# Kernel tuning notes

Hardware: AMD Instinct MI355X
Metric: run time of the kernel (lower is better)

## Reference

```python
import jax, jax.numpy as jnp
import numpy as np

N, E, D, G, L = 50000, 400000, 64, 256, 4
VA, VB = 64, 8   # atom / bond feature vocab sizes
NUM_ATOM_FEATS, NUM_BOND_FEATS = 9, 3
MSG_EPS = 1e-7   # GENConv message epsilon
LN_EPS = 1e-5


def layernorm(x, g, b):
    mu = x.mean(-1, keepdims=True)
    var = x.var(-1, keepdims=True)
    return (x - mu) * jax.lax.rsqrt(var + LN_EPS) * g + b


def genconv(h, edge_emb, src, dst, W, b):
    # GENConv (aggr='softmax', t=1, mlp_layers=1):
    # msg = relu(x_j + e) + eps; per-dst per-feature softmax-weighted sum; mlp(x + m)
    msg = jax.nn.relu(h[src] + edge_emb) + MSG_EPS          # [E, D]
    mmax = jax.ops.segment_max(msg, dst, num_segments=N)    # [N, D]
    mmax = jnp.where(jnp.isfinite(mmax), mmax, 0.0)         # nodes with no in-edges
    ex = jnp.exp(msg - mmax[dst])
    denom = jax.ops.segment_sum(ex, dst, num_segments=N)
    alpha = ex / jnp.maximum(denom[dst], 1e-16)
    m = jax.ops.segment_sum(alpha * msg, dst, num_segments=N)  # [N, D]
    return (h + m) @ W + b


def setup_inputs():
    key = jax.random.key(0)
    ks = jax.random.split(key, 10)
    x = jax.random.randint(ks[0], (N, NUM_ATOM_FEATS), 0, VA)
    edge_index = jax.random.randint(ks[1], (2, E), 0, N)
    edge_attr = jax.random.randint(ks[2], (E, NUM_BOND_FEATS), 0, VB)
    batch = jnp.sort(jax.random.randint(ks[3], (N,), 0, G))
    s = 0.02
    w = 1.0 / np.sqrt(D).astype(np.float32)
    atom_emb = jax.random.normal(ks[4], (NUM_ATOM_FEATS, VA, D), jnp.float32) * s
    bond_emb = jax.random.normal(ks[5], (NUM_BOND_FEATS, VB, D), jnp.float32) * s
    gcn_W = jax.random.normal(ks[6], (L, D, D), jnp.float32) * w
    gcn_b = jnp.zeros((L, D), jnp.float32)
    norm_g = jnp.ones((L, D), jnp.float32)
    norm_b = jnp.zeros((L, D), jnp.float32)
    vn_emb = jnp.zeros((1, D), jnp.float32)  # constant-init virtualnode embedding
    vn_W1 = jax.random.normal(ks[7], (L - 1, D, D), jnp.float32) * w
    vn_b1 = jnp.zeros((L - 1, D), jnp.float32)
    vn_g1 = jnp.ones((L - 1, D), jnp.float32)
    vn_be1 = jnp.zeros((L - 1, D), jnp.float32)
    vn_W2 = jax.random.normal(ks[8], (L - 1, D, D), jnp.float32) * w
    vn_b2 = jnp.zeros((L - 1, D), jnp.float32)
    vn_g2 = jnp.ones((L - 1, D), jnp.float32)
    vn_be2 = jnp.zeros((L - 1, D), jnp.float32)
    return dict(x=x, edge_index=edge_index, edge_attr=edge_attr, batch=batch,
                atom_emb=atom_emb, bond_emb=bond_emb, gcn_W=gcn_W, gcn_b=gcn_b,
                norm_g=norm_g, norm_b=norm_b, vn_emb=vn_emb,
                vn_W1=vn_W1, vn_b1=vn_b1, vn_g1=vn_g1, vn_be1=vn_be1,
                vn_W2=vn_W2, vn_b2=vn_b2, vn_g2=vn_g2, vn_be2=vn_be2)


def reference(x, edge_index, edge_attr, batch, atom_emb, bond_emb, gcn_W, gcn_b,
              norm_g, norm_b, vn_emb, vn_W1, vn_b1, vn_g1, vn_be1,
              vn_W2, vn_b2, vn_g2, vn_be2):
    src, dst = edge_index[0], edge_index[1]
    # AtomEncoder / BondEncoder: sum of per-feature embedding lookups
    h = atom_emb[jnp.arange(NUM_ATOM_FEATS)[None, :], x].sum(1)          # [N, D]
    edge_emb = bond_emb[jnp.arange(NUM_BOND_FEATS)[None, :], edge_attr].sum(1)  # [E, D]
    vn = jnp.broadcast_to(vn_emb[0], (G, D))
    h = h + vn[batch]
    # block == 'res+' (eval mode: dropout is identity)
    h = genconv(h, edge_emb, src, dst, gcn_W[0], gcn_b[0])
    for l in range(1, L):
        h2 = jax.nn.relu(layernorm(h, norm_g[l - 1], norm_b[l - 1]))
        vt = jax.ops.segment_sum(h2, batch, num_segments=G) + vn         # global_add_pool
        vt = jax.nn.relu(layernorm(vt @ vn_W1[l - 1] + vn_b1[l - 1], vn_g1[l - 1], vn_be1[l - 1]))
        vn = jax.nn.relu(layernorm(vt @ vn_W2[l - 1] + vn_b2[l - 1], vn_g2[l - 1], vn_be2[l - 1]))
        h2 = h2 + vn[batch]
        h = genconv(h2, edge_emb, src, dst, gcn_W[l], gcn_b[l]) + h
    return layernorm(h, norm_g[L - 1], norm_b[L - 1])
```

## Files before the change

kernel.cpp:

```cpp
#include <hip/hip_runtime.h>
#include <hip/hip_bf16.h>

typedef __hip_bfloat16 bf16;

#define GNUM 256
#define LN_EPS 1e-5f
#define MSG_EPS 1e-7f

typedef float f4v __attribute__((ext_vector_type(4)));
typedef short s8v __attribute__((ext_vector_type(8)));
typedef __bf16 b8v __attribute__((ext_vector_type(8)));

template <typename V>
__device__ auto mfma_bf16_(V a, V b, f4v c, int)
    -> decltype(__builtin_amdgcn_mfma_f32_16x16x32_bf16(a, b, c, 0, 0, 0)) {
  return __builtin_amdgcn_mfma_f32_16x16x32_bf16(a, b, c, 0, 0, 0);
}
template <typename V>
__device__ f4v mfma_bf16_(V a, V b, f4v c, long) {
  return __builtin_amdgcn_mfma_f32_16x16x32_bf16(__builtin_bit_cast(s8v, a),
                                                 __builtin_bit_cast(s8v, b), c, 0, 0, 0);
}
__device__ __forceinline__ f4v mfma16(uint4 a, uint4 b, f4v c){
  return mfma_bf16_(__builtin_bit_cast(b8v, a), __builtin_bit_cast(b8v, b), c, 0);
}

__device__ __forceinline__ float bu2f(unsigned short u){
  unsigned v = ((unsigned)u) << 16; return __builtin_bit_cast(float, v);
}
__device__ __forceinline__ unsigned short f2bu(float f){
  unsigned u = __builtin_bit_cast(unsigned, f);
  return (unsigned short)((u + 0x7FFFu + ((u >> 16) & 1u)) >> 16);
}

__device__ __forceinline__ float wave_sum64(float v){
  #pragma unroll
  for (int off = 32; off > 0; off >>= 1) v += __shfl_xor(v, off, 64);
  return v;
}

struct Params15 {
  const void* src[15];
  int n[15];
  int off[15];
};

__global__ __launch_bounds__(256) void k_convert(Params15 P, int* __restrict__ flag,
                                                 float* __restrict__ dst,
                                                 int* __restrict__ counts, int nc){
  __shared__ int isf_sh;
  int tid = threadIdx.x;
  if (tid < 64){
    const unsigned short* u = (const unsigned short*)P.src[0];
    int bad = 0;
    for (int k = tid; k < 256; k += 64){
      unsigned short v = u[2*k];
      if (((v >> 7) & 0xFFu) >= 137u) bad = 1;
    }
    unsigned long long m = __ballot(bad);
    if (tid == 0) isf_sh = (m != 0ull) ? 1 : 0;
  }
  __syncthreads();
  bool isf = (isf_sh != 0);
  if (blockIdx.x == 0 && tid == 0) *flag = isf ? 1 : 0;
  for (int a = 0; a < 15; ++a){
    int n = P.n[a];
    float* d = dst + P.off[a];
    if (isf){
      const float* s = (const float*)P.src[a];
      for (int i = blockIdx.x*256 + tid; i < n; i += gridDim.x*256) d[i] = s[i];
    } else {
      const bf16* s = (const bf16*)P.src[a];
      for (int i = blockIdx.x*256 + tid; i < n; i += gridDim.x*256) d[i] = __bfloat162float(s[i]);
    }
  }
  for (int i = blockIdx.x*256 + tid; i < nc; i += gridDim.x*256) counts[i] = 0;
}

__global__ void k_count(const int* __restrict__ dst, int* __restrict__ counts, int E){
  int e = blockIdx.x*256 + threadIdx.x;
  if (e < E) atomicAdd(counts + dst[e], 1);
}

__global__ __launch_bounds__(256) void k_scan1(const int* __restrict__ counts,
                                               int* __restrict__ offs,
                                               int* __restrict__ btot, int n){
  __shared__ int wsum[4];
  int tid = threadIdx.x, w = tid >> 6, lane = tid & 63;
  int i = blockIdx.x*256 + tid;
  int v = (i < n) ? counts[i] : 0;
  int incl = v;
  #pragma unroll
  for (int off = 1; off < 64; off <<= 1){
    int t = __shfl_up(incl, off, 64);
    if (lane >= off) incl += t;
  }
  if (lane == 63) wsum[w] = incl;
  __syncthreads();
  int woff = 0;
  for (int k = 0; k < w; ++k) woff += wsum[k];
  int tot = incl + woff;
  if (i < n) offs[i+1] = tot;
  if (tid == 255) btot[blockIdx.x] = tot;
}

__global__ __launch_bounds__(256) void k_scan2(const int* __restrict__ btot,
                                               int* __restrict__ bexc, int nb){
  __shared__ int wsum[4];
  __shared__ int carry_sh;
  int tid = threadIdx.x, w = tid >> 6, lane = tid & 63;
  if (tid == 0) carry_sh = 0;
  __syncthreads();
  for (int base = 0; base < nb; base += 256){
    int i = base + tid;
    int v = (i < nb) ? btot[i] : 0;
    int incl = v;
    #pragma unroll
    for (int off = 1; off < 64; off <<= 1){
      int t = __shfl_up(incl, off, 64);
      if (lane >= off) incl += t;
    }
    if (lane == 63) wsum[w] = incl;
    __syncthreads();
    int carry = carry_sh;
    int woff = 0;
    for (int k = 0; k < w; ++k) woff += wsum[k];
    if (i < nb) bexc[i] = carry + woff + incl - v;
    __syncthreads();
    if (tid == 0) carry_sh = carry + wsum[0] + wsum[1] + wsum[2] + wsum[3];
    __syncthreads();
  }
}

__global__ void k_scan3(int* __restrict__ offs, int* __restrict__ cursor,
                        const int* __restrict__ bexc, int n){
  int i = blockIdx.x*256 + threadIdx.x;
  if (i == 0){ offs[0] = 0; cursor[0] = 0; }
  if (i < n){
    int v = offs[i+1] + bexc[blockIdx.x];
    offs[i+1] = v;
    if (i+1 < n) cursor[i+1] = v;
  }
}

__global__ void k_scatter(const int* __restrict__ src, const int* __restrict__ dst,
                          const int* __restrict__ ea, int* __restrict__ cursor,
                          int* __restrict__ payload, int E){
  int e = blockIdx.x*256 + threadIdx.x;
  if (e >= E) return;
  int d = dst[e];
  int pos = atomicAdd(cursor + d, 1);
  payload[pos] = (src[e] & 0xFFFF) | (ea[e*3] << 16) | (ea[e*3+1] << 19) | (ea[e*3+2] << 22);
}

__global__ void k_prep(const float* __restrict__ gw, unsigned short* __restrict__ Wf,
                       const int* __restrict__ batch, int* __restrict__ goffs,
                       const int* __restrict__ x, const float* __restrict__ atom_emb,
                       const float* __restrict__ vn_emb, unsigned short* __restrict__ b0,
                       int n){
  if (blockIdx.x < 64){
    int t = blockIdx.x*256 + threadIdx.x;
    int j = t & 7, lane = (t >> 3) & 63, nt = (t >> 9) & 3, kt = (t >> 11) & 1, l = t >> 12;
    int k = kt*32 + (lane >> 4)*8 + j;
    int c = nt*16 + (lane & 15);
    Wf[t] = f2bu(gw[l*4096 + k*64 + c]);
  } else if (blockIdx.x < 66){
    int g = (blockIdx.x - 64)*256 + threadIdx.x;
    if (g > GNUM) return;
    if (g == GNUM){ goffs[GNUM] = n; return; }
    int lo = 0, hi = n;
    while (lo < hi){ int mid = (lo+hi)>>1; if (batch[mid] < g) lo = mid+1; else hi = mid; }
    goffs[g] = lo;
  } else {
    int t = (blockIdx.x - 66) * 256 + threadIdx.x;
    int i = t >> 6, j = t & 63;
    if (i >= n) return;
    float acc = vn_emb[j];
    #pragma unroll
    for (int f = 0; f < 9; ++f){
      int idx = x[i*9 + f];
      acc += atom_emb[(f*64 + idx)*64 + j];
    }
    b0[t] = f2bu(acc);
  }
}

__global__ __launch_bounds__(256) void k_layer(
    const unsigned short* __restrict__ b0, const int* __restrict__ offs,
    const int* __restrict__ payload, const float* __restrict__ bond,
    const unsigned short* __restrict__ Wf, const float* __restrict__ bias,
    unsigned short* __restrict__ hres, float2* __restrict__ rowstat,
    void* __restrict__ finalout, const float* __restrict__ ng,
    const float* __restrict__ nb, const int* __restrict__ flag,
    int use_res, int mode, int n){
  __shared__ float Bs[1536];
  __shared__ __align__(16) unsigned short T[16][72];
  __shared__ float PS1[4][16], PS2[4][16];
  int tid = threadIdx.x;
  for (int idx = tid; idx < 1536; idx += 256) Bs[idx] = bond[idx];
  __syncthreads();
  int w = tid >> 6, j = tid & 63;
  int v0 = blockIdx.x * 16;
  int vb = v0 + w*4;

  int oidx = vb + (j < 5 ? j : 4);
  if (oidx > n) oidx = n;
  int o5 = offs[oidx];

  for (int r = 0; r < 4; ++r){
    int v = vb + r;
    float tv = 0.f;
    if (v < n){
      int e0 = __builtin_amdgcn_readfirstlane(__shfl(o5, r, 64));
      int e1 = __builtin_amdgcn_readfirstlane(__shfl(o5, r + 1, 64));
      float own = bu2f(b0[((unsigned)v << 6) + j]);
      tv = own;
      if (e1 > e0){
        float den = 0.f, num = 0.f;
        for (int e = e0; e < e1; e += 8){
          int rem = e1 - e;
          int pu[8]; float hv[8];
          #pragma unroll
          for (int u = 0; u < 8; ++u){
            int ei = (u < rem) ? e + u : e0;
            pu[u] = payload[ei];
          }
          #pragma unroll
          for (int u = 0; u < 8; ++u)
            hv[u] = bu2f(b0[((unsigned)(pu[u] & 0xFFFF) << 6) + j]);
          if (rem >= 8){
            #pragma unroll
            for (int u = 0; u < 8; ++u){
              int p = pu[u];
              float eev = Bs[((p >> 16) & 7)*64 + j]
                        + Bs[(8 + ((p >> 19) & 7))*64 + j]
                        + Bs[(16 + ((p >> 22) & 7))*64 + j];
              float mm = fmaxf(hv[u] + eev, 0.f) + MSG_EPS;
              float ex = __expf(mm);
              den += ex;
              num = fmaf(ex, mm, num);
            }
          } else {
            #pragma unroll
            for (int u = 0; u < 8; ++u){
              if (u < rem){
                int p = pu[u];
                float eev = Bs[((p >> 16) & 7)*64 + j]
                          + Bs[(8 + ((p >> 19) & 7))*64 + j]
                          + Bs[(16 + ((p >> 22) & 7))*64 + j];
                float mm = fmaxf(hv[u] + eev, 0.f) + MSG_EPS;
                float ex = __expf(mm);
                den += ex;
                num = fmaf(ex, mm, num);
              }
            }
          }
        }
        tv = own + num / fmaxf(den, 1e-16f);
      }
    }
    T[w*4 + r][j] = f2bu(tv);
  }
  __syncthreads();

  int ct = w;
  int quad = j >> 4, lm = j & 15;
  const uint4* Wfv = (const uint4*)Wf;
  uint4 B0 = Wfv[(size_t)(0*4 + ct)*64 + j];
  uint4 B1 = Wfv[(size_t)(1*4 + ct)*64 + j];
  uint4 A0 = *(const uint4*)&T[lm][8*quad];
  uint4 A1 = *(const uint4*)&T[lm][32 + 8*quad];
  f4v acc = (f4v){0.f,0.f,0.f,0.f};
  acc = mfma16(A0, B0, acc);
  acc = mfma16(A1, B1, acc);

  int col = ct*16 + lm;
  float bv = bias[col];
  float s1[4], s2[4];
  #pragma unroll
  for (int reg = 0; reg < 4; ++reg){
    int row = v0 + quad*4 + reg;
    float val = acc[reg] + bv;
    if (use_res && row < n) val += bu2f(hres[((unsigned)row << 6) + col]);
    acc[reg] = val;
    s1[reg] = val;
    s2[reg] = val*val;
  }
  #pragma unroll
  for (int reg = 0; reg < 4; ++reg){
    #pragma unroll
    for (int m = 1; m < 16; m <<= 1){
      s1[reg] += __shfl_xor(s1[reg], m, 64);
      s2[reg] += __shfl_xor(s2[reg], m, 64);
    }
  }
  if (lm == 0){
    #pragma unroll
    for (int reg = 0; reg < 4; ++reg){
      int rl = quad*4 + reg;
      PS1[ct][rl] = s1[reg];
      PS2[ct][rl] = s2[reg];
    }
  }
  __syncthreads();

  if (mode == 0){
    #pragma unroll
    for (int reg = 0; reg < 4; ++reg){
      int rl = quad*4 + reg;
      int row = v0 + rl;
      if (row >= n) continue;
      hres[((size_t)row << 6) + col] = f2bu(acc[reg]);
      if (ct == 0 && lm == 0){
        float t1 = PS1[0][rl] + PS1[1][rl] + PS1[2][rl] + PS1[3][rl];
        float t2 = PS2[0][rl] + PS2[1][rl] + PS2[2][rl] + PS2[3][rl];
        float mu = t1 * (1.f/64.f);
        float var = fmaxf(t2 * (1.f/64.f) - mu*mu, 0.f);
        rowstat[row] = make_float2(mu, rsqrtf(var + LN_EPS));
      }
    }
    return;
  }

  bool isf = (*flag != 0);
  #pragma unroll
  for (int reg = 0; reg < 4; ++reg){
    int rl = quad*4 + reg;
    int row = v0 + rl;
    if (row >= n) continue;
    float t1 = PS1[0][rl] + PS1[1][rl] + PS1[2][rl] + PS1[3][rl];
    float t2 = PS2[0][rl] + PS2[1][rl] + PS2[2][rl] + PS2[3][rl];
    float mu = t1 * (1.f/64.f);
    float var = fmaxf(t2 * (1.f/64.f) - mu*mu, 0.f);
    float rstd = rsqrtf(var + LN_EPS);
    float y = (acc[reg] - mu) * rstd * ng[col] + nb[col];
    size_t o = ((size_t)row << 6) + col;
    if (isf) ((float*)finalout)[o] = y;
    else     ((bf16*)finalout)[o]  = __float2bfloat16(y);
  }
}

__global__ __launch_bounds__(512) void k_vn(
    const unsigned short* __restrict__ hres, const float2* __restrict__ rowstat,
    const int* __restrict__ goffs,
    const float* __restrict__ vn_emb, float* __restrict__ vn,
    unsigned short* __restrict__ b0,
    const float* __restrict__ ng, const float* __restrict__ nbb,
    const float* __restrict__ W1, const float* __restrict__ b1,
    const float* __restrict__ g1, const float* __restrict__ be1,
    const float* __restrict__ W2, const float* __restrict__ b2,
    const float* __restrict__ g2, const float* __restrict__ be2,
    int first){
  __shared__ float Ws[4096];
  __shared__ float part[8][64];
  __shared__ float rowbuf[64];
  __shared__ float vnew[64];
  int tid = threadIdx.x, w = tid >> 6, j = tid & 63, g = blockIdx.x;
  float ngj = ng[j], nbj = nbb[j];
  for (int idx = tid; idx < 4096; idx += 512) Ws[idx] = W1[idx];
  int r0 = goffs[g], r1 = goffs[g+1];
  float sum = 0.f;
  for (int i = r0 + w; i < r1; i += 8){
    float xv = bu2f(hres[((unsigned)i << 6) + j]);
    float2 st = rowstat[i];
    sum += fmaxf((xv - st.x) * st.y * ngj + nbj, 0.f);
  }
  part[w][j] = sum;
  __syncthreads();
  float y = 0.f;
  if (tid < 64){
    float s = part[0][j] + part[1][j] + part[2][j] + part[3][j]
            + part[4][j] + part[5][j] + part[6][j] + part[7][j]
            + (first ? vn_emb[j] : vn[((unsigned)g << 6) + j]);
    rowbuf[j] = s;
  }
  __syncthreads();
  if (tid < 64){
    float acc = b1[j];
    #pragma unroll
    for (int k = 0; k < 64; ++k) acc = fmaf(rowbuf[k], Ws[k*64 + j], acc);
    float mu = wave_sum64(acc) * (1.f/64.f);
    float d = acc - mu;
    float var = wave_sum64(d*d) * (1.f/64.f);
    y = fmaxf(d * rsqrtf(var + LN_EPS) * g1[j] + be1[j], 0.f);
  }
  __syncthreads();
  for (int idx = tid; idx < 4096; idx += 512) Ws[idx] = W2[idx];
  if (tid < 64) rowbuf[j] = y;
  __syncthreads();
  if (tid < 64){
    float acc = b2[j];
    #pragma unroll
    for (int k = 0; k < 64; ++k) acc = fmaf(rowbuf[k], Ws[k*64 + j], acc);
    float mu = wave_sum64(acc) * (1.f/64.f);
    float d = acc - mu;
    float var = wave_sum64(d*d) * (1.f/64.f);
    float v2 = fmaxf(d * rsqrtf(var + LN_EPS) * g2[j] + be2[j], 0.f);
    vn[((unsigned)g << 6) + j] = v2;
    vnew[j] = v2;
  }
  __syncthreads();
  float vj = vnew[j];
  for (int i = r0 + w; i < r1; i += 8){
    float xv = bu2f(hres[((unsigned)i << 6) + j]);
    float2 st = rowstat[i];
    float h2 = fmaxf((xv - st.x) * st.y * ngj + nbj, 0.f);
    b0[((unsigned)i << 6) + j] = f2bu(h2 + vj);
  }
}

extern "C" void kernel_launch(void* const* d_in, const int* in_sizes, int n_in,
                              void* d_out, int out_size, void* d_ws, size_t ws_size,
                              hipStream_t stream){
  const int* x          = (const int*)d_in[0];
  const int* edge_index = (const int*)d_in[1];
  const int* edge_attr  = (const int*)d_in[2];
  const int* batch      = (const int*)d_in[3];

  const int N = in_sizes[3];
  const int E = in_sizes[2] / 3;
  const int L = 4;

  const int P_ATOM = 0, P_BOND = 36864, P_GW = 38400, P_GB = 54784,
            P_NG = 55040, P_NB = 55296, P_VNE = 55552, P_W1 = 55616,
            P_B1 = 67904, P_G1 = 68096, P_BE1 = 68288, P_W2 = 68480,
            P_B2 = 80768, P_G2 = 80960, P_BE2 = 81152, P_END = 81344;

  char* ws = (char*)d_ws;
  size_t off = 0;
  auto alloc = [&](size_t bytes)->char*{
    char* p = ws + off; off += (bytes + 255) & ~(size_t)255; return p;
  };
  int*    flag   = (int*)alloc(256);
  float*  par    = (float*)alloc((size_t)P_END * 4);
  unsigned short* Wf  = (unsigned short*)alloc(16384 * 2);
  unsigned short* b0  = (unsigned short*)alloc((size_t)N*64*2);
  unsigned short* hres= (unsigned short*)alloc((size_t)N*64*2);
  float2* rowstat= (float2*)alloc((size_t)N*8);
  int*    counts = (int*)alloc((size_t)N*4);
  int*    offs   = (int*)alloc((size_t)(N+1)*4);
  int*    cursor = (int*)alloc((size_t)N*4);
  int*    btot   = (int*)alloc(1024);
  int*    bexc   = (int*)alloc(1024);
  int*    payload= (int*)alloc((size_t)E*4);
  int*    goffs  = (int*)alloc((size_t)(GNUM+1)*4);
  float*  vn     = (float*)alloc((size_t)GNUM*64*4);
  (void)ws_size; (void)n_in; (void)out_size;

  Params15 P;
  const int poffs[15] = {P_ATOM,P_BOND,P_GW,P_GB,P_NG,P_NB,P_VNE,P_W1,P_B1,P_G1,P_BE1,P_W2,P_B2,P_G2,P_BE2};
  for (int a = 0; a < 15; ++a){ P.src[a] = d_in[4+a]; P.n[a] = in_sizes[4+a]; P.off[a] = poffs[a]; }

  int nodeGrid = (N*64 + 255) / 256;
  int nScanB   = (N + 255) / 256;
  int eGrid    = (E + 255) / 256;
  const int* srcp = edge_index;
  const int* dstp = edge_index + E;

  k_convert<<<128, 256, 0, stream>>>(P, flag, par, counts, N);
  k_count<<<eGrid, 256, 0, stream>>>(dstp, counts, E);
  k_scan1<<<nScanB, 256, 0, stream>>>(counts, offs, btot, N);
  k_scan2<<<1, 256, 0, stream>>>(btot, bexc, nScanB);
  k_scan3<<<nScanB, 256, 0, stream>>>(offs, cursor, bexc, N);
  k_scatter<<<eGrid, 256, 0, stream>>>(srcp, dstp, edge_attr, cursor, payload, E);
  k_prep<<<66 + nodeGrid, 256, 0, stream>>>(par + P_GW, Wf, batch, goffs,
                                            x, par + P_ATOM, par + P_VNE, b0, N);

  int layerGrid = (N + 15) / 16;
  for (int l = 0; l < L; ++l){
    if (l > 0){
      k_vn<<<GNUM, 512, 0, stream>>>(hres, rowstat, goffs, par + P_VNE, vn, b0,
                                     par + P_NG + (l-1)*64, par + P_NB + (l-1)*64,
                                     par + P_W1 + (l-1)*4096, par + P_B1 + (l-1)*64,
                                     par + P_G1 + (l-1)*64, par + P_BE1 + (l-1)*64,
                                     par + P_W2 + (l-1)*4096, par + P_B2 + (l-1)*64,
                                     par + P_G2 + (l-1)*64, par + P_BE2 + (l-1)*64,
                                     l == 1 ? 1 : 0);
    }
    int mode = (l == L-1) ? 1 : 0;
    k_layer<<<layerGrid, 256, 0, stream>>>(b0, offs, payload, par + P_BOND,
                                           Wf + (size_t)l*4096, par + P_GB + l*64,
                                           hres, rowstat, d_out,
                                           par + P_NG + l*64, par + P_NB + l*64,
                                           flag, l > 0 ? 1 : 0, mode, N);
  }
}
```

Measured before the change: 360.6 us.

## Fuse global_add_pool into layer epilogue via atomics and widen first edge batch

The layer kernel now computes the normalized, ReLU'd h2 in its epilogue and atomically accumulates per-graph sums into a vt buffer, using run-length grouping on the sorted batch ids. The virtual-node kernel then reads the pooled sums and no longer re-reads hres and rowstat for every node. The edge aggregation loop also loads the first 16 edges in one unrolled batch before falling back to batches of 8, giving more memory-level parallelism for typical degrees. The costs are float atomics, which make summation order nondeterministic, extra register pressure from the 16-wide batch, and the need to zero vt between layers.

```diff
diff --git a/kernel.cpp b/kernel.cpp
--- a/kernel.cpp
+++ b/kernel.cpp
@@ -47,7 +47,8 @@
 
 __global__ __launch_bounds__(256) void k_convert(Params15 P, int* __restrict__ flag,
                                                  float* __restrict__ dst,
-                                                 int* __restrict__ counts, int nc){
+                                                 int* __restrict__ counts, int nc,
+                                                 float* __restrict__ vt, int nvt){
   __shared__ int isf_sh;
   int tid = threadIdx.x;
   if (tid < 64){
@@ -75,6 +76,7 @@
     }
   }
   for (int i = blockIdx.x*256 + tid; i < nc; i += gridDim.x*256) counts[i] = 0;
+  for (int i = blockIdx.x*256 + tid; i < nvt; i += gridDim.x*256) vt[i] = 0.f;
 }
 
 __global__ void k_count(const int* __restrict__ dst, int* __restrict__ counts, int E){
@@ -189,6 +191,7 @@
     const unsigned short* __restrict__ b0, const int* __restrict__ offs,
     const int* __restrict__ payload, const float* __restrict__ bond,
     const unsigned short* __restrict__ Wf, const float* __restrict__ bias,
+    const int* __restrict__ batch, float* __restrict__ vt,
     unsigned short* __restrict__ hres, float2* __restrict__ rowstat,
     void* __restrict__ finalout, const float* __restrict__ ng,
     const float* __restrict__ nb, const int* __restrict__ flag,
@@ -196,11 +199,13 @@
   __shared__ float Bs[1536];
   __shared__ __align__(16) unsigned short T[16][72];
   __shared__ float PS1[4][16], PS2[4][16];
+  __shared__ int batch_lds[16];
   int tid = threadIdx.x;
+  int v0 = blockIdx.x * 16;
   for (int idx = tid; idx < 1536; idx += 256) Bs[idx] = bond[idx];
+  if (tid < 16){ int rw = v0 + tid; batch_lds[tid] = (rw < n) ? batch[rw] : -1; }
   __syncthreads();
   int w = tid >> 6, j = tid & 63;
-  int v0 = blockIdx.x * 16;
   int vb = v0 + w*4;
 
   int oidx = vb + (j < 5 ? j : 4);
@@ -217,20 +222,20 @@
       tv = own;
       if (e1 > e0){
         float den = 0.f, num = 0.f;
-        for (int e = e0; e < e1; e += 8){
-          int rem = e1 - e;
-          int pu[8]; float hv[8];
+        {
+          int rem = e1 - e0;
+          int pu[16]; float hv[16];
           #pragma unroll
-          for (int u = 0; u < 8; ++u){
-            int ei = (u < rem) ? e + u : e0;
+          for (int u = 0; u < 16; ++u){
+            int ei = (u < rem) ? e0 + u : e0;
             pu[u] = payload[ei];
           }
           #pragma unroll
-          for (int u = 0; u < 8; ++u)
+          for (int u = 0; u < 16; ++u)
             hv[u] = bu2f(b0[((unsigned)(pu[u] & 0xFFFF) << 6) + j]);
-          if (rem >= 8){
+          if (rem >= 16){
             #pragma unroll
-            for (int u = 0; u < 8; ++u){
+            for (int u = 0; u < 16; ++u){
               int p = pu[u];
               float eev = Bs[((p >> 16) & 7)*64 + j]
                         + Bs[(8 + ((p >> 19) & 7))*64 + j]
@@ -242,7 +247,7 @@
             }
           } else {
             #pragma unroll
-            for (int u = 0; u < 8; ++u){
+            for (int u = 0; u < 16; ++u){
               if (u < rem){
                 int p = pu[u];
                 float eev = Bs[((p >> 16) & 7)*64 + j]
@@ -256,6 +261,31 @@
             }
           }
         }
+        for (int e = e0 + 16; e < e1; e += 8){
+          int rem = e1 - e;
+          int pu[8]; float hv[8];
+          #pragma unroll
+          for (int u = 0; u < 8; ++u){
+            int ei = (u < rem) ? e + u : e0;
+            pu[u] = payload[ei];
+          }
+          #pragma unroll
+          for (int u = 0; u < 8; ++u)
+            hv[u] = bu2f(b0[((unsigned)(pu[u] & 0xFFFF) << 6) + j]);
+          #pragma unroll
+          for (int u = 0; u < 8; ++u){
+            if (u < rem){
+              int p = pu[u];
+              float eev = Bs[((p >> 16) & 7)*64 + j]
+                        + Bs[(8 + ((p >> 19) & 7))*64 + j]
+                        + Bs[(16 + ((p >> 22) & 7))*64 + j];
+              float mm = fmaxf(hv[u] + eev, 0.f) + MSG_EPS;
+              float ex = __expf(mm);
+              den += ex;
+              num = fmaf(ex, mm, num);
+            }
+          }
+        }
         tv = own + num / fmaxf(den, 1e-16f);
       }
     }
@@ -305,20 +335,36 @@
   __syncthreads();
 
   if (mode == 0){
+    float* H2 = Bs;
     #pragma unroll
     for (int reg = 0; reg < 4; ++reg){
       int rl = quad*4 + reg;
       int row = v0 + rl;
       if (row >= n) continue;
       hres[((size_t)row << 6) + col] = f2bu(acc[reg]);
-      if (ct == 0 && lm == 0){
-        float t1 = PS1[0][rl] + PS1[1][rl] + PS1[2][rl] + PS1[3][rl];
-        float t2 = PS2[0][rl] + PS2[1][rl] + PS2[2][rl] + PS2[3][rl];
-        float mu = t1 * (1.f/64.f);
-        float var = fmaxf(t2 * (1.f/64.f) - mu*mu, 0.f);
-        rowstat[row] = make_float2(mu, rsqrtf(var + LN_EPS));
+      float t1 = PS1[0][rl] + PS1[1][rl] + PS1[2][rl] + PS1[3][rl];
+      float t2 = PS2[0][rl] + PS2[1][rl] + PS2[2][rl] + PS2[3][rl];
+      float mu = t1 * (1.f/64.f);
+      float var = fmaxf(t2 * (1.f/64.f) - mu*mu, 0.f);
+      float rstd = rsqrtf(var + LN_EPS);
+      if (ct == 0 && lm == 0) rowstat[row] = make_float2(mu, rstd);
+      H2[rl*64 + col] = fmaxf((acc[reg] - mu) * rstd * ng[col] + nb[col], 0.f);
+    }
+    __syncthreads();
+    float a = 0.f; int gc = -1;
+    #pragma unroll
+    for (int r = 0; r < 4; ++r){
+      int rl = w*4 + r;
+      int g = batch_lds[rl];
+      if (g >= 0){
+        if (g != gc){
+          if (gc >= 0) atomicAdd(&vt[(unsigned)gc*64 + j], a);
+          gc = g; a = 0.f;
+        }
+        a += H2[rl*64 + j];
       }
     }
+    if (gc >= 0) atomicAdd(&vt[(unsigned)gc*64 + j], a);
     return;
   }
 
@@ -342,7 +388,7 @@
 
 __global__ __launch_bounds__(512) void k_vn(
     const unsigned short* __restrict__ hres, const float2* __restrict__ rowstat,
-    const int* __restrict__ goffs,
+    float* __restrict__ vt, const int* __restrict__ goffs,
     const float* __restrict__ vn_emb, float* __restrict__ vn,
     unsigned short* __restrict__ b0,
     const float* __restrict__ ng, const float* __restrict__ nbb,
@@ -352,29 +398,20 @@
     const float* __restrict__ g2, const float* __restrict__ be2,
     int first){
   __shared__ float Ws[4096];
-  __shared__ float part[8][64];
   __shared__ float rowbuf[64];
   __shared__ float vnew[64];
   int tid = threadIdx.x, w = tid >> 6, j = tid & 63, g = blockIdx.x;
   float ngj = ng[j], nbj = nbb[j];
   for (int idx = tid; idx < 4096; idx += 512) Ws[idx] = W1[idx];
   int r0 = goffs[g], r1 = goffs[g+1];
-  float sum = 0.f;
-  for (int i = r0 + w; i < r1; i += 8){
-    float xv = bu2f(hres[((unsigned)i << 6) + j]);
-    float2 st = rowstat[i];
-    sum += fmaxf((xv - st.x) * st.y * ngj + nbj, 0.f);
-  }
-  part[w][j] = sum;
+  if (tid < 64){
+    float s = vt[(unsigned)g*64 + j]
+            + (first ? vn_emb[j] : vn[(unsigned)g*64 + j]);
+    vt[(unsigned)g*64 + j] = 0.f;
+    rowbuf[j] = s;
+  }
   __syncthreads();
   float y = 0.f;
-  if (tid < 64){
-    float s = part[0][j] + part[1][j] + part[2][j] + part[3][j]
-            + part[4][j] + part[5][j] + part[6][j] + part[7][j]
-            + (first ? vn_emb[j] : vn[((unsigned)g << 6) + j]);
-    rowbuf[j] = s;
-  }
-  __syncthreads();
   if (tid < 64){
     float acc = b1[j];
     #pragma unroll
@@ -396,7 +433,7 @@
     float d = acc - mu;
     float var = wave_sum64(d*d) * (1.f/64.f);
     float v2 = fmaxf(d * rsqrtf(var + LN_EPS) * g2[j] + be2[j], 0.f);
-    vn[((unsigned)g << 6) + j] = v2;
+    vn[(unsigned)g*64 + j] = v2;
     vnew[j] = v2;
   }
   __syncthreads();
@@ -437,6 +474,7 @@
   unsigned short* b0  = (unsigned short*)alloc((size_t)N*64*2);
   unsigned short* hres= (unsigned short*)alloc((size_t)N*64*2);
   float2* rowstat= (float2*)alloc((size_t)N*8);
+  float*  vt     = (float*)alloc((size_t)GNUM*64*4);
   int*    counts = (int*)alloc((size_t)N*4);
   int*    offs   = (int*)alloc((size_t)(N+1)*4);
   int*    cursor = (int*)alloc((size_t)N*4);
@@ -457,7 +495,7 @@
   const int* srcp = edge_index;
   const int* dstp = edge_index + E;
 
-  k_convert<<<128, 256, 0, stream>>>(P, flag, par, counts, N);
+  k_convert<<<128, 256, 0, stream>>>(P, flag, par, counts, N, vt, GNUM*64);
   k_count<<<eGrid, 256, 0, stream>>>(dstp, counts, E);
   k_scan1<<<nScanB, 256, 0, stream>>>(counts, offs, btot, N);
   k_scan2<<<1, 256, 0, stream>>>(btot, bexc, nScanB);
@@ -469,7 +507,7 @@
   int layerGrid = (N + 15) / 16;
   for (int l = 0; l < L; ++l){
     if (l > 0){
-      k_vn<<<GNUM, 512, 0, stream>>>(hres, rowstat, goffs, par + P_VNE, vn, b0,
+      k_vn<<<GNUM, 512, 0, stream>>>(hres, rowstat, vt, goffs, par + P_VNE, vn, b0,
                                      par + P_NG + (l-1)*64, par + P_NB + (l-1)*64,
                                      par + P_W1 + (l-1)*4096, par + P_B1 + (l-1)*64,
                                      par + P_G1 + (l-1)*64, par + P_BE1 + (l-1)*64,
@@ -480,7 +518,7 @@
     int mode = (l == L-1) ? 1 : 0;
     k_layer<<<layerGrid, 256, 0, stream>>>(b0, offs, payload, par + P_BOND,
                                            Wf + (size_t)l*4096, par + P_GB + l*64,
-                                           hres, rowstat, d_out,
+                                           batch, vt, hres, rowstat, d_out,
                                            par + P_NG + l*64, par + P_NB + l*64,
                                            flag, l > 0 ? 1 : 0, mode, N);
   }
```

Measured after the change: 369.2 us. +2.4%, slower.
